# Optimization experiments

Measured on AMD Instinct MI355X. Metric: run time of the kernel, lower is better.

Reference implementation:

```python
import jax, jax.numpy as jnp
import numpy as np

D_MODEL = 2048
N_HEADS = 16
D_HEAD = D_MODEL // N_HEADS
B, S = 4, 2048


def setup_inputs() -> dict:
    key = jax.random.key(0)
    ks = jax.random.split(key, 5)
    scale = 1.0 / np.sqrt(D_MODEL)
    return {
        "x": jax.random.normal(ks[0], (B, S, D_MODEL), dtype=jnp.float32),
        "w_qkv": jax.random.normal(ks[1], (D_MODEL, 3 * D_MODEL), dtype=jnp.float32) * scale,
        "b_qkv": jax.random.normal(ks[2], (3 * D_MODEL,), dtype=jnp.float32) * 0.01,
        "w_out": jax.random.normal(ks[3], (D_MODEL, D_MODEL), dtype=jnp.float32) * scale,
        "b_out": jax.random.normal(ks[4], (D_MODEL,), dtype=jnp.float32) * 0.01,
    }


def reference(x, w_qkv, b_qkv, w_out, b_out):
    b, s, d = x.shape
    qkv = x @ w_qkv + b_qkv                      # [b, s, 3d]
    q, k, v = jnp.split(qkv, 3, axis=-1)
    # [b, h, s, dh]
    q = q.reshape(b, s, N_HEADS, D_HEAD).transpose(0, 2, 1, 3)
    k = k.reshape(b, s, N_HEADS, D_HEAD).transpose(0, 2, 1, 3)
    v = v.reshape(b, s, N_HEADS, D_HEAD).transpose(0, 2, 1, 3)
    # past_kv is None -> s_past == s
    scale = 1.0 / np.sqrt(D_HEAD).astype(np.float32)
    scores = jnp.einsum("bhqd,bhkd->bhqk", q, k) * scale  # [b, h, s, s]
    # causal mask: disallow j > i (diagonal = 1 + s_past - s = 1)
    causal = jnp.tril(jnp.ones((s, s), dtype=bool))
    scores = jnp.where(causal, scores, jnp.float32(-jnp.inf))
    attn = jax.nn.softmax(scores, axis=-1)
    out = jnp.einsum("bhqk,bhkd->bhqd", attn, v)          # [b, h, s, dh]
    out = out.transpose(0, 2, 1, 3).reshape(b, s, d)
    out = out @ w_out + b_out
    return out, k, v
```

## Files before the change

### kernel.cpp

```cpp
#include <hip/hip_runtime.h>
#include <hip/hip_bf16.h>
#include <cstdint>

typedef unsigned short u16;
typedef unsigned int u32;
typedef __attribute__((ext_vector_type(4))) float f32x4;
typedef __attribute__((ext_vector_type(8))) __bf16 bf16x8;

#define DEVFN static __device__ __forceinline__

constexpr int Bb = 4, S = 2048, Dm = 2048, H = 16, DH = 128;
constexpr int M  = Bb * S;
constexpr int N3 = 3 * Dm;
constexpr float ATTN_SCALE = 0.088388347648318447f;
constexpr float LOG2E = 1.4426950408889634f;

DEVFN u16 f2bf(float f) {
  union { float f; u32 u; } v; v.f = f;
  u32 u = v.u;
  return (u16)((u + 0x7fffu + ((u >> 16) & 1u)) >> 16);
}

DEVFN void async16(const void* g, void* l) {
  __builtin_amdgcn_global_load_lds(
      (__attribute__((address_space(1))) unsigned int*)(g),
      (__attribute__((address_space(3))) unsigned int*)(l), 16, 0, 0);
}


__global__ __launch_bounds__(256) void k_cvt_bf16(const float* __restrict__ in,
                                                  u16* __restrict__ out, int n) {
  int i = (blockIdx.x * 256 + threadIdx.x) * 4;
  if (i < n) {
    float4 f = *(const float4*)(in + i);
    ushort4 o;
    o.x = f2bf(f.x); o.y = f2bf(f.y); o.z = f2bf(f.z); o.w = f2bf(f.w);
    *(ushort4*)(out + i) = o;
  }
}

__global__ __launch_bounds__(256) void k_transpose_bf16(const float* __restrict__ in,
                                                        u16* __restrict__ out,
                                                        int R, int C) {
  __shared__ float tile[32][33];
  int c0 = blockIdx.x * 32, r0 = blockIdx.y * 32;
  int tx = threadIdx.x & 31, ty = threadIdx.x >> 5;
#pragma unroll
  for (int i = 0; i < 4; i++)
    tile[ty + 8 * i][tx] = in[(size_t)(r0 + ty + 8 * i) * C + c0 + tx];
  __syncthreads();
#pragma unroll
  for (int i = 0; i < 4; i++)
    out[(size_t)(c0 + ty + 8 * i) * R + r0 + tx] = f2bf(tile[tx][ty + 8 * i]);
}


#define RA(buf, half) ((buf) * 65536 + (half) * 16384)
#define RB(buf, half) ((buf) * 65536 + 32768 + (half) * 16384)

DEVFN void stage_half(const u16* __restrict__ g, int grow0, int K, int vtile,
                      char* lds, int region, int tid) {
#pragma unroll
  for (int j = 0; j < 2; j++) {
    int L = j * 8192 + tid * 16;
    int row = L >> 7;
    int col = (((L & 127) ^ ((row & 7) << 4)) >> 1) + vtile * 64;
    async16(g + (size_t)(grow0 + row) * K + col,
            lds + region + j * 8192 + (tid & ~63) * 16);
  }
}

template <int BUF, int MSUB>
DEVFN void ldA(const char* lds, int wm, int lrow, int lkg, bf16x8 af[4][2]) {
#pragma unroll
  for (int mi = 0; mi < 4; mi++)
#pragma unroll
    for (int kk = 0; kk < 2; kk++) {
      int row = MSUB * 64 + mi * 16 + lrow;
      af[mi][kk] = *(const bf16x8*)(lds + RA(BUF, 0) + wm * 16384 + row * 128 +
                                    ((kk * 64 + lkg * 16) ^ ((row & 7) << 4)));
    }
}

template <int BUF, int NSUB>
DEVFN void ldB(const char* lds, int wn, int lrow, int lkg, bf16x8 bfr[2][2]) {
#pragma unroll
  for (int ni = 0; ni < 2; ni++)
#pragma unroll
    for (int kk = 0; kk < 2; kk++) {
      int row = (wn & 1) * 64 + NSUB * 32 + ni * 16 + lrow;
      bfr[ni][kk] = *(const bf16x8*)(lds + RB(BUF, 0) + (wn >> 1) * 16384 +
                                     row * 128 +
                                     ((kk * 64 + lkg * 16) ^ ((row & 7) << 4)));
    }
}

template <int MSUB, int NSUB>
DEVFN void mmq(f32x4 acc[8][4], bf16x8 af[4][2], bf16x8 bfr[2][2]) {
  __builtin_amdgcn_s_setprio(1);
#pragma unroll
  for (int kk = 0; kk < 2; kk++)
#pragma unroll
    for (int mi = 0; mi < 4; mi++)
#pragma unroll
      for (int ni = 0; ni < 2; ni++)
        acc[MSUB * 4 + mi][NSUB * 2 + ni] = __builtin_amdgcn_mfma_f32_16x16x32_bf16(
            af[mi][kk], bfr[ni][kk], acc[MSUB * 4 + mi][NSUB * 2 + ni], 0, 0, 0);
  __builtin_amdgcn_s_setprio(0);
}

#define BARRIER() __builtin_amdgcn_s_barrier()
#define LGK0() asm volatile("s_waitcnt lgkmcnt(0)" ::: "memory")
#define VM4() asm volatile("s_waitcnt vmcnt(4)" ::: "memory")

template <int MODE>
__global__ __launch_bounds__(512, 2) void k_gemm(
    const u16* __restrict__ A, const u16* __restrict__ BT,
    const float* __restrict__ bias, float* __restrict__ Cf,
    u16* __restrict__ q_bf, u16* __restrict__ k_bf, u16* __restrict__ v_bfT,
    int K, int N) {
  __shared__ __align__(16) char lds[131072];
  const int tid = threadIdx.x;
  const int wid = tid >> 6, lane = tid & 63;
  const int wm = wid >> 2, wn = wid & 3;
  const int lrow = lane & 15, lkg = lane >> 4;

  const int bid = blockIdx.x;
  const int xcd = bid & 7;
  const int i = bid >> 3;
  const int r = i & 15;
  const int j = i >> 4;
  const int tm0 = (xcd * 4 + (r >> 2)) << 8;
  const int tn0 = (j * 4 + (r & 3)) << 8;

  const int NT = K >> 6;

  f32x4 acc[8][4] = {};

  stage_half(A, tm0,       K, 0, lds, RA(0, 0), tid);
  stage_half(BT, tn0,      K, 0, lds, RB(0, 0), tid);
  stage_half(A, tm0 + 128, K, 0, lds, RA(0, 1), tid);
  stage_half(BT, tn0 + 128,K, 0, lds, RB(0, 1), tid);
  stage_half(A, tm0,       K, 1, lds, RA(1, 0), tid);
  stage_half(BT, tn0,      K, 1, lds, RB(1, 0), tid);
  VM4();
  BARRIER();

  for (int u = 0; u < NT; u += 2) {
    const int v2 = (u + 2 < NT) ? u + 2 : 0;
    const int v3 = (u + 3 < NT) ? u + 3 : 0;
    bf16x8 af[4][2], b0[2][2], b1[2][2];

    ldA<0, 0>(lds, wm, lrow, lkg, af);
    ldB<0, 0>(lds, wn, lrow, lkg, b0);
    stage_half(BT, tn0 + 128, K, u + 1, lds, RB(1, 1), tid);
    BARRIER(); LGK0();
    mmq<0, 0>(acc, af, b0);
    BARRIER();

    ldB<0, 1>(lds, wn, lrow, lkg, b1);
    stage_half(A, tm0 + 128, K, u + 1, lds, RA(1, 1), tid);
    BARRIER(); LGK0();
    mmq<0, 1>(acc, af, b1);
    BARRIER();

    ldA<0, 1>(lds, wm, lrow, lkg, af);
    stage_half(BT, tn0, K, v2, lds, RB(0, 0), tid);
    BARRIER(); LGK0();
    mmq<1, 0>(acc, af, b0);
    BARRIER();

    stage_half(A, tm0, K, v2, lds, RA(0, 0), tid);
    VM4();
    BARRIER();
    mmq<1, 1>(acc, af, b1);
    BARRIER();

    ldA<1, 0>(lds, wm, lrow, lkg, af);
    ldB<1, 0>(lds, wn, lrow, lkg, b0);
    stage_half(A, tm0 + 128, K, v2, lds, RA(0, 1), tid);
    BARRIER(); LGK0();
    mmq<0, 0>(acc, af, b0);
    BARRIER();

    ldB<1, 1>(lds, wn, lrow, lkg, b1);
    stage_half(BT, tn0 + 128, K, v2, lds, RB(0, 1), tid);
    BARRIER(); LGK0();
    mmq<0, 1>(acc, af, b1);
    BARRIER();

    ldA<1, 1>(lds, wm, lrow, lkg, af);
    stage_half(BT, tn0, K, v3, lds, RB(1, 0), tid);
    BARRIER(); LGK0();
    mmq<1, 0>(acc, af, b0);
    BARRIER();

    stage_half(A, tm0, K, v3, lds, RA(1, 0), tid);
    VM4();
    BARRIER();
    mmq<1, 1>(acc, af, b1);
    BARRIER();
  }

  if (MODE == 0) {
#pragma unroll
    for (int mig = 0; mig < 8; mig++) {
      int row = tm0 + wm * 128 + (mig >> 2) * 64 + (mig & 3) * 16 + lkg * 4;
#pragma unroll
      for (int nig = 0; nig < 4; nig++) {
        int col = tn0 + wn * 64 + (nig >> 1) * 32 + (nig & 1) * 16 + lrow;
        float bv = bias[col];
#pragma unroll
        for (int r2 = 0; r2 < 4; r2++)
          Cf[(size_t)(row + r2) * N + col] = acc[mig][nig][r2] + bv;
      }
    }
  } else {
#pragma unroll
    for (int mig = 0; mig < 8; mig++) {
      int row = tm0 + wm * 128 + (mig >> 2) * 64 + (mig & 3) * 16 + lkg * 4;
#pragma unroll
      for (int nig = 0; nig < 4; nig++) {
        int n = tn0 + wn * 64 + (nig >> 1) * 32 + (nig & 1) * 16 + lrow;
        float bv = bias[n];
        int type = n >> 11;
        int d = n & 2047;
        int h = d >> 7, dh = d & 127;
#pragma unroll
        for (int r2 = 0; r2 < 4; r2++) {
          int rr = row + r2;
          int b = rr >> 11, s = rr & 2047;
          float val = acc[mig][nig][r2] + bv;
          size_t idx = ((size_t)(b * H + h) * S + s) * DH + dh;
          if (type == 0) {
            q_bf[idx] = f2bf(val * ATTN_SCALE);
          } else if (type == 1) {
            Cf[(size_t)M * Dm + idx] = val;
            k_bf[idx] = f2bf(val);
          } else {
            Cf[(size_t)2 * M * Dm + idx] = val;
            v_bfT[((size_t)(b * H + h) * DH + dh) * S + s] = f2bf(val);
          }
        }
      }
    }
  }
}

__global__ __launch_bounds__(256, 2) void k_attn(const u16* __restrict__ q_bf,
                                                 const u16* __restrict__ k_bf,
                                                 const u16* __restrict__ v_bfT,
                                                 u16* __restrict__ attn_bf) {
  __shared__ u16 ldsK[2][64 * 128];
  __shared__ u16 ldsV[2][128 * 64];
  __shared__ u16 ldsP[4][32 * 64];

  const int tid = threadIdx.x;
  const int wid = tid >> 6, lane = tid & 63;
  const int lrow = lane & 15, lkg = lane >> 4;

  const int bid = blockIdx.x;
  const int xcd = bid & 7;
  const int ii = bid >> 3;
  const int bh = xcd * 8 + (ii >> 4);
  const int qi = 15 - (ii & 15);
  const int b = bh >> 4, h = bh & 15;
  const int wq0 = qi * 128 + wid * 32;
  const int swz = (lrow & 7) << 4;

  const u16* qp = q_bf + (size_t)bh * S * DH;
  const u16* kp = k_bf + (size_t)bh * S * DH;
  const u16* vp = v_bfT + (size_t)bh * DH * S;

  bf16x8 qf[2][4];
#pragma unroll
  for (int qt = 0; qt < 2; qt++)
#pragma unroll
    for (int kk = 0; kk < 4; kk++)
      qf[qt][kk] = *(const bf16x8*)(qp + (size_t)(wq0 + qt * 16 + lrow) * DH +
                                    kk * 32 + lkg * 8);

  float mr[2][4], lr[2][4];
#pragma unroll
  for (int qt = 0; qt < 2; qt++)
#pragma unroll
    for (int r = 0; r < 4; r++) { mr[qt][r] = -1e30f; lr[qt][r] = 0.f; }
  f32x4 oacc[2][8] = {};

  const int nkb = qi * 2 + 2;

  auto stage = [&](int kb, int buf) {
#pragma unroll
    for (int i = 0; i < 4; i++) {
      int L = i * 4096 + wid * 1024 + lane * 16;
      int krow = L >> 8, kch = (L >> 4) & 15;
      async16(kp + (size_t)(kb * 64 + krow) * DH + ((kch ^ (krow & 7)) * 8),
              (char*)ldsK[buf] + L);
      int vd = L >> 7, vch = (L >> 4) & 7;
      async16(vp + (size_t)vd * S + kb * 64 + ((vch ^ (vd & 7)) * 8),
              (char*)ldsV[buf] + L);
    }
  };

  stage(0, 0);
  asm volatile("s_waitcnt vmcnt(0)" ::: "memory");
  __builtin_amdgcn_s_barrier();

  int cur = 0;
  for (int kb = 0; kb < nkb; kb++) {
    if (kb + 1 < nkb) stage(kb + 1, cur ^ 1);

    if (kb * 64 <= wq0 + 31) {
      const u16* Kc = ldsK[cur];
      const u16* Vc = ldsV[cur];
      f32x4 sacc[2][4] = {};
      __builtin_amdgcn_s_setprio(1);
#pragma unroll
      for (int kt = 0; kt < 4; kt++)
#pragma unroll
        for (int kk = 0; kk < 4; kk++) {
          bf16x8 kf = *(const bf16x8*)((const char*)Kc +
                        (kt * 16 + lrow) * 256 + ((kk * 64 + lkg * 16) ^ swz));
          sacc[0][kt] = __builtin_amdgcn_mfma_f32_16x16x32_bf16(qf[0][kk], kf,
                                                                sacc[0][kt], 0, 0, 0);
          sacc[1][kt] = __builtin_amdgcn_mfma_f32_16x16x32_bf16(qf[1][kk], kf,
                                                                sacc[1][kt], 0, 0, 0);
        }
      __builtin_amdgcn_s_setprio(0);

      if (kb * 64 + 63 > wq0) {
#pragma unroll
        for (int qt = 0; qt < 2; qt++)
#pragma unroll
          for (int kt = 0; kt < 4; kt++) {
            int k = kb * 64 + kt * 16 + lrow;
#pragma unroll
            for (int r = 0; r < 4; r++)
              if (k > wq0 + qt * 16 + lkg * 4 + r) sacc[qt][kt][r] = -1e30f;
          }
      }

      float pm[2][4];
#pragma unroll
      for (int qt = 0; qt < 2; qt++)
#pragma unroll
        for (int r = 0; r < 4; r++)
          pm[qt][r] = fmaxf(fmaxf(sacc[qt][0][r], sacc[qt][1][r]),
                            fmaxf(sacc[qt][2][r], sacc[qt][3][r]));
#pragma unroll
      for (int off = 1; off < 16; off <<= 1)
#pragma unroll
        for (int qt = 0; qt < 2; qt++)
#pragma unroll
          for (int r = 0; r < 4; r++)
            pm[qt][r] = fmaxf(pm[qt][r], __shfl_xor(pm[qt][r], off, 64));

      float dmax = pm[0][0] - mr[0][0];
#pragma unroll
      for (int qt = 0; qt < 2; qt++)
#pragma unroll
        for (int r = 0; r < 4; r++)
          dmax = fmaxf(dmax, pm[qt][r] - mr[qt][r]);
      if (!__all(dmax <= 8.0f)) {
        float sc[2][4];
#pragma unroll
        for (int qt = 0; qt < 2; qt++)
#pragma unroll
          for (int r = 0; r < 4; r++) {
            float mn = fmaxf(mr[qt][r], pm[qt][r]);
            sc[qt][r] = exp2f((mr[qt][r] - mn) * LOG2E);
            mr[qt][r] = mn;
            lr[qt][r] *= sc[qt][r];
          }
#pragma unroll
        for (int qt = 0; qt < 2; qt++)
#pragma unroll
          for (int nd = 0; nd < 8; nd++)
#pragma unroll
            for (int r = 0; r < 4; r++) oacc[qt][nd][r] *= sc[qt][r];
      }

      float rs[2][4] = {};
#pragma unroll
      for (int qt = 0; qt < 2; qt++)
#pragma unroll
        for (int kt = 0; kt < 4; kt++)
#pragma unroll
          for (int r = 0; r < 4; r++) {
            float p = exp2f((sacc[qt][kt][r] - mr[qt][r]) * LOG2E);
            rs[qt][r] += p;
            int prow = qt * 16 + lkg * 4 + r;
            *(u16*)((char*)ldsP[wid] + prow * 128 +
                    (((kt * 16 + lrow) * 2) ^ ((prow & 7) << 4))) = f2bf(p);
          }
#pragma unroll
      for (int off = 1; off < 16; off <<= 1)
#pragma unroll
        for (int qt = 0; qt < 2; qt++)
#pragma unroll
          for (int r = 0; r < 4; r++)
            rs[qt][r] += __shfl_xor(rs[qt][r], off, 64);
#pragma unroll
      for (int qt = 0; qt < 2; qt++)
#pragma unroll
        for (int r = 0; r < 4; r++)
          lr[qt][r] += rs[qt][r];

      asm volatile("s_waitcnt lgkmcnt(0)" ::: "memory");
      bf16x8 pf[2][2];
#pragma unroll
      for (int qt = 0; qt < 2; qt++)
#pragma unroll
        for (int kk = 0; kk < 2; kk++)
          pf[qt][kk] = *(const bf16x8*)((const char*)ldsP[wid] +
                         (qt * 16 + lrow) * 128 + ((kk * 64 + lkg * 16) ^ swz));
      __builtin_amdgcn_s_setprio(1);
#pragma unroll
      for (int nd = 0; nd < 8; nd++) {
        bf16x8 vf0 = *(const bf16x8*)((const char*)Vc +
                       (nd * 16 + lrow) * 128 + ((lkg * 16) ^ swz));
        bf16x8 vf1 = *(const bf16x8*)((const char*)Vc +
                       (nd * 16 + lrow) * 128 + ((64 + lkg * 16) ^ swz));
#pragma unroll
        for (int qt = 0; qt < 2; qt++) {
          oacc[qt][nd] = __builtin_amdgcn_mfma_f32_16x16x32_bf16(pf[qt][0], vf0,
                                                                 oacc[qt][nd], 0, 0, 0);
          oacc[qt][nd] = __builtin_amdgcn_mfma_f32_16x16x32_bf16(pf[qt][1], vf1,
                                                                 oacc[qt][nd], 0, 0, 0);
        }
      }
      __builtin_amdgcn_s_setprio(0);
    }

    asm volatile("s_waitcnt vmcnt(0)" ::: "memory");
    __builtin_amdgcn_s_barrier();
    cur ^= 1;
  }

#pragma unroll
  for (int qt = 0; qt < 2; qt++) {
    float inv[4];
#pragma unroll
    for (int r = 0; r < 4; r++) inv[r] = 1.0f / lr[qt][r];
#pragma unroll
    for (int nd = 0; nd < 8; nd++)
#pragma unroll
      for (int r = 0; r < 4; r++) {
        int q = wq0 + qt * 16 + lkg * 4 + r;
        size_t idx = ((size_t)(b * S + q) * H + h) * DH + nd * 16 + lrow;
        attn_bf[idx] = f2bf(oacc[qt][nd][r] * inv[r]);
      }
  }
}


extern "C" void kernel_launch(void* const* d_in, const int* in_sizes, int n_in,
                              void* d_out, int out_size, void* d_ws, size_t ws_size,
                              hipStream_t stream) {
  const float* x     = (const float*)d_in[0];
  const float* w_qkv = (const float*)d_in[1];
  const float* b_qkv = (const float*)d_in[2];
  const float* w_out = (const float*)d_in[3];
  const float* b_out = (const float*)d_in[4];
  float* out = (float*)d_out;

  char* ws = (char*)d_ws;
  u16* x_bf    = (u16*)ws; ws += (size_t)M * Dm * 2;
  u16* wqkvT   = (u16*)ws; ws += (size_t)N3 * Dm * 2;
  u16* woutT   = (u16*)ws; ws += (size_t)Dm * Dm * 2;
  u16* q_bf    = (u16*)ws; ws += (size_t)M * Dm * 2;
  u16* k_bf    = (u16*)ws; ws += (size_t)M * Dm * 2;
  u16* v_bfT   = (u16*)ws; ws += (size_t)M * Dm * 2;
  u16* attn_bf = (u16*)ws; ws += (size_t)M * Dm * 2;

  k_cvt_bf16<<<(M * Dm) / 1024, 256, 0, stream>>>(x, x_bf, M * Dm);
  k_transpose_bf16<<<dim3(N3 / 32, Dm / 32), 256, 0, stream>>>(w_qkv, wqkvT, Dm, N3);
  k_transpose_bf16<<<dim3(Dm / 32, Dm / 32), 256, 0, stream>>>(w_out, woutT, Dm, Dm);

  k_gemm<1><<<(N3 / 256) * (M / 256), 512, 0, stream>>>(
      x_bf, wqkvT, b_qkv, out, q_bf, k_bf, v_bfT, Dm, N3);

  k_attn<<<S / 128 * Bb * H, 256, 0, stream>>>(q_bf, k_bf, v_bfT, attn_bf);

  k_gemm<0><<<(Dm / 256) * (M / 256), 512, 0, stream>>>(
      attn_bf, woutT, b_out, out, nullptr, nullptr, nullptr, Dm, Dm);
}
```

Measured before the change: 549.9 us.

## Restructure GEMM main loop with hoisted A fragments and pointer-increment staging

The GEMM main loop now loads both A sub-tiles from LDS once per buffer instead of twice. It uses precomputed per-thread global pointers that advance by 64 elements, replacing per-call address math. K is fixed at compile time, prologue staging is reordered with a deeper vmcnt wait, and the out-of-range wraparound prefetch is removed in favour of a final vmcnt(0) drain. The goal is fewer LDS reads and less integer address overhead, at the cost of more registers for A fragments and a late prefetch that may read past the tile end.

Measured after the change: 559.9 us. No clear change (+1.8%).

```diff
diff --git a/kernel.cpp b/kernel.cpp
--- a/kernel.cpp
+++ b/kernel.cpp
@@ -12,6 +12,7 @@
 constexpr int Bb = 4, S = 2048, Dm = 2048, H = 16, DH = 128;
 constexpr int M  = Bb * S;
 constexpr int N3 = 3 * Dm;
+constexpr int KK = 2048;
 constexpr float ATTN_SCALE = 0.088388347648318447f;
 constexpr float LOG2E = 1.4426950408889634f;
 
@@ -58,68 +59,71 @@
 #define RA(buf, half) ((buf) * 65536 + (half) * 16384)
 #define RB(buf, half) ((buf) * 65536 + 32768 + (half) * 16384)
 
-DEVFN void stage_half(const u16* __restrict__ g, int grow0, int K, int vtile,
-                      char* lds, int region, int tid) {
-#pragma unroll
-  for (int j = 0; j < 2; j++) {
-    int L = j * 8192 + tid * 16;
-    int row = L >> 7;
-    int col = (((L & 127) ^ ((row & 7) << 4)) >> 1) + vtile * 64;
-    async16(g + (size_t)(grow0 + row) * K + col,
-            lds + region + j * 8192 + (tid & ~63) * 16);
-  }
-}
-
-template <int BUF, int MSUB>
-DEVFN void ldA(const char* lds, int wm, int lrow, int lkg, bf16x8 af[4][2]) {
-#pragma unroll
-  for (int mi = 0; mi < 4; mi++)
-#pragma unroll
-    for (int kk = 0; kk < 2; kk++) {
-      int row = MSUB * 64 + mi * 16 + lrow;
-      af[mi][kk] = *(const bf16x8*)(lds + RA(BUF, 0) + wm * 16384 + row * 128 +
-                                    ((kk * 64 + lkg * 16) ^ ((row & 7) << 4)));
-    }
-}
-
-template <int BUF, int NSUB>
-DEVFN void ldB(const char* lds, int wn, int lrow, int lkg, bf16x8 bfr[2][2]) {
-#pragma unroll
-  for (int ni = 0; ni < 2; ni++)
-#pragma unroll
-    for (int kk = 0; kk < 2; kk++) {
-      int row = (wn & 1) * 64 + NSUB * 32 + ni * 16 + lrow;
-      bfr[ni][kk] = *(const bf16x8*)(lds + RB(BUF, 0) + (wn >> 1) * 16384 +
-                                     row * 128 +
-                                     ((kk * 64 + lkg * 16) ^ ((row & 7) << 4)));
-    }
-}
-
-template <int MSUB, int NSUB>
-DEVFN void mmq(f32x4 acc[8][4], bf16x8 af[4][2], bf16x8 bfr[2][2]) {
-  __builtin_amdgcn_s_setprio(1);
-#pragma unroll
-  for (int kk = 0; kk < 2; kk++)
-#pragma unroll
-    for (int mi = 0; mi < 4; mi++)
-#pragma unroll
-      for (int ni = 0; ni < 2; ni++)
-        acc[MSUB * 4 + mi][NSUB * 2 + ni] = __builtin_amdgcn_mfma_f32_16x16x32_bf16(
-            af[mi][kk], bfr[ni][kk], acc[MSUB * 4 + mi][NSUB * 2 + ni], 0, 0, 0);
-  __builtin_amdgcn_s_setprio(0);
-}
-
 #define BARRIER() __builtin_amdgcn_s_barrier()
 #define LGK0() asm volatile("s_waitcnt lgkmcnt(0)" ::: "memory")
-#define VM4() asm volatile("s_waitcnt vmcnt(4)" ::: "memory")
+#define VM6() asm volatile("s_waitcnt vmcnt(6)" ::: "memory")
+#define VM0() asm volatile("s_waitcnt vmcnt(0)" ::: "memory")
+
+template <int BUF>
+DEVFN void ldAall(const char* lds, int wm, int lrow, int lkg, bf16x8 af[2][4][2]) {
+  const char* base = lds + RA(BUF, 0) + wm * 16384;
+  const int sw = (lrow & 7) << 4;
+#pragma unroll
+  for (int ms = 0; ms < 2; ms++)
+#pragma unroll
+    for (int mi = 0; mi < 4; mi++) {
+      int row = ms * 64 + mi * 16 + lrow;
+#pragma unroll
+      for (int kk = 0; kk < 2; kk++)
+        af[ms][mi][kk] = *(const bf16x8*)(base + row * 128 +
+                                          ((kk * 64 + lkg * 16) ^ sw));
+    }
+}
+
+template <int BUF, int NS>
+DEVFN void ldB(const char* lds, int wn, int lrow, int lkg, bf16x8 b[2][2]) {
+  const char* base = lds + RB(BUF, 0) + (wn >> 1) * 16384;
+  const int sw = (lrow & 7) << 4;
+#pragma unroll
+  for (int ni = 0; ni < 2; ni++) {
+    int row = (wn & 1) * 64 + NS * 32 + ni * 16 + lrow;
+#pragma unroll
+    for (int kk = 0; kk < 2; kk++)
+      b[ni][kk] = *(const bf16x8*)(base + row * 128 +
+                                   ((kk * 64 + lkg * 16) ^ sw));
+  }
+}
+
+template <int MS, int NS>
+DEVFN void mmq(f32x4 acc[8][4], bf16x8 af[4][2], bf16x8 b[2][2]) {
+  __builtin_amdgcn_s_setprio(1);
+#pragma unroll
+  for (int kk = 0; kk < 2; kk++)
+#pragma unroll
+    for (int mi = 0; mi < 4; mi++)
+#pragma unroll
+      for (int ni = 0; ni < 2; ni++)
+        acc[MS * 4 + mi][NS * 2 + ni] = __builtin_amdgcn_mfma_f32_16x16x32_bf16(
+            af[mi][kk], b[ni][kk], acc[MS * 4 + mi][NS * 2 + ni], 0, 0, 0);
+  __builtin_amdgcn_s_setprio(0);
+}
+
+#define STAGE0(ptr, region)                                             \
+  {                                                                     \
+    const u16* _q = (ptr);                                              \
+    async16(_q, ldsc + (region) + dstoff);                              \
+    async16(_q + (size_t)64 * KK, ldsc + (region) + 8192 + dstoff);     \
+  }
+#define STAGE(p, region) { STAGE0(p, region); p += 64; }
 
 template <int MODE>
 __global__ __launch_bounds__(512, 2) void k_gemm(
     const u16* __restrict__ A, const u16* __restrict__ BT,
     const float* __restrict__ bias, float* __restrict__ Cf,
     u16* __restrict__ q_bf, u16* __restrict__ k_bf, u16* __restrict__ v_bfT,
-    int K, int N) {
+    int N) {
   __shared__ __align__(16) char lds[131072];
+  char* ldsc = lds;
   const int tid = threadIdx.x;
   const int wid = tid >> 6, lane = tid & 63;
   const int wm = wid >> 2, wn = wid & 3;
@@ -133,74 +137,85 @@
   const int tm0 = (xcd * 4 + (r >> 2)) << 8;
   const int tn0 = (j * 4 + (r & 3)) << 8;
 
-  const int NT = K >> 6;
+  const int NT = KK >> 6;
+
+  const int srow = tid >> 3;
+  const int scol = (((tid & 7) * 16) ^ ((srow & 7) << 4)) >> 1;
+  const int dstoff = (tid & ~63) * 16;
+  const u16* bA0 = A + (size_t)(tm0 + srow) * KK + scol;
+  const u16* bA1 = A + (size_t)(tm0 + 128 + srow) * KK + scol;
+  const u16* bB0 = BT + (size_t)(tn0 + srow) * KK + scol;
+  const u16* bB1 = BT + (size_t)(tn0 + 128 + srow) * KK + scol;
 
   f32x4 acc[8][4] = {};
 
-  stage_half(A, tm0,       K, 0, lds, RA(0, 0), tid);
-  stage_half(BT, tn0,      K, 0, lds, RB(0, 0), tid);
-  stage_half(A, tm0 + 128, K, 0, lds, RA(0, 1), tid);
-  stage_half(BT, tn0 + 128,K, 0, lds, RB(0, 1), tid);
-  stage_half(A, tm0,       K, 1, lds, RA(1, 0), tid);
-  stage_half(BT, tn0,      K, 1, lds, RB(1, 0), tid);
-  VM4();
+  STAGE0(bA0, RA(0, 0));
+  STAGE0(bA1, RA(0, 1));
+  STAGE0(bB0, RB(0, 0));
+  STAGE0(bB1, RB(0, 1));
+  STAGE0(bA0 + 64, RA(1, 0));
+  STAGE0(bA1 + 64, RA(1, 1));
+  STAGE0(bB0 + 64, RB(1, 0));
+  VM6();
   BARRIER();
 
-  for (int u = 0; u < NT; u += 2) {
-    const int v2 = (u + 2 < NT) ? u + 2 : 0;
-    const int v3 = (u + 3 < NT) ? u + 3 : 0;
-    bf16x8 af[4][2], b0[2][2], b1[2][2];
-
-    ldA<0, 0>(lds, wm, lrow, lkg, af);
-    ldB<0, 0>(lds, wn, lrow, lkg, b0);
-    stage_half(BT, tn0 + 128, K, u + 1, lds, RB(1, 1), tid);
+  const u16* pB1 = bB1 + 64;
+  const u16* pA0 = bA0 + 128;
+  const u16* pA1 = bA1 + 128;
+  const u16* pB0 = bB0 + 128;
+
+  for (int it = 0; it < NT / 2; it++) {
+    bf16x8 af[2][4][2], b0[2][2], b1[2][2];
+
+    ldAall<0>(ldsc, wm, lrow, lkg, af);
+    ldB<0, 0>(ldsc, wn, lrow, lkg, b0);
+    STAGE(pB1, RB(1, 1));
     BARRIER(); LGK0();
-    mmq<0, 0>(acc, af, b0);
-    BARRIER();
-
-    ldB<0, 1>(lds, wn, lrow, lkg, b1);
-    stage_half(A, tm0 + 128, K, u + 1, lds, RA(1, 1), tid);
+    mmq<0, 0>(acc, af[0], b0);
+    BARRIER();
+
+    ldB<0, 1>(ldsc, wn, lrow, lkg, b1);
+    STAGE(pA0, RA(0, 0));
     BARRIER(); LGK0();
-    mmq<0, 1>(acc, af, b1);
-    BARRIER();
-
-    ldA<0, 1>(lds, wm, lrow, lkg, af);
-    stage_half(BT, tn0, K, v2, lds, RB(0, 0), tid);
+    mmq<0, 1>(acc, af[0], b1);
+    BARRIER();
+
+    STAGE(pA1, RA(0, 1));
+    BARRIER();
+    mmq<1, 0>(acc, af[1], b0);
+    BARRIER();
+
+    STAGE(pB0, RB(0, 0));
+    VM6();
+    BARRIER();
+    mmq<1, 1>(acc, af[1], b1);
+    BARRIER();
+
+    ldAall<1>(ldsc, wm, lrow, lkg, af);
+    ldB<1, 0>(ldsc, wn, lrow, lkg, b0);
+    STAGE(pB1, RB(0, 1));
     BARRIER(); LGK0();
-    mmq<1, 0>(acc, af, b0);
-    BARRIER();
-
-    stage_half(A, tm0, K, v2, lds, RA(0, 0), tid);
-    VM4();
-    BARRIER();
-    mmq<1, 1>(acc, af, b1);
-    BARRIER();
-
-    ldA<1, 0>(lds, wm, lrow, lkg, af);
-    ldB<1, 0>(lds, wn, lrow, lkg, b0);
-    stage_half(A, tm0 + 128, K, v2, lds, RA(0, 1), tid);
+    mmq<0, 0>(acc, af[0], b0);
+    BARRIER();
+
+    ldB<1, 1>(ldsc, wn, lrow, lkg, b1);
+    STAGE(pA0, RA(1, 0));
     BARRIER(); LGK0();
-    mmq<0, 0>(acc, af, b0);
-    BARRIER();
-
-    ldB<1, 1>(lds, wn, lrow, lkg, b1);
-    stage_half(BT, tn0 + 128, K, v2, lds, RB(0, 1), tid);
-    BARRIER(); LGK0();
-    mmq<0, 1>(acc, af, b1);
-    BARRIER();
-
-    ldA<1, 1>(lds, wm, lrow, lkg, af);
-    stage_half(BT, tn0, K, v3, lds, RB(1, 0), tid);
-    BARRIER(); LGK0();
-    mmq<1, 0>(acc, af, b0);
-    BARRIER();
-
-    stage_half(A, tm0, K, v3, lds, RA(1, 0), tid);
-    VM4();
-    BARRIER();
-    mmq<1, 1>(acc, af, b1);
-    BARRIER();
-  }
+    mmq<0, 1>(acc, af[0], b1);
+    BARRIER();
+
+    STAGE(pA1, RA(1, 1));
+    BARRIER();
+    mmq<1, 0>(acc, af[1], b0);
+    BARRIER();
+
+    STAGE(pB0, RB(1, 0));
+    VM6();
+    BARRIER();
+    mmq<1, 1>(acc, af[1], b1);
+    BARRIER();
+  }
+  VM0();
 
   if (MODE == 0) {
 #pragma unroll
@@ -478,10 +493,10 @@
   k_transpose_bf16<<<dim3(Dm / 32, Dm / 32), 256, 0, stream>>>(w_out, woutT, Dm, Dm);
 
   k_gemm<1><<<(N3 / 256) * (M / 256), 512, 0, stream>>>(
-      x_bf, wqkvT, b_qkv, out, q_bf, k_bf, v_bfT, Dm, N3);
+      x_bf, wqkvT, b_qkv, out, q_bf, k_bf, v_bfT, N3);
 
   k_attn<<<S / 128 * Bb * H, 256, 0, stream>>>(q_bf, k_bf, v_bfT, attn_bf);
 
   k_gemm<0><<<(Dm / 256) * (M / 256), 512, 0, stream>>>(
-      attn_bf, woutT, b_out, out, nullptr, nullptr, nullptr, Dm, Dm);
-}
+      attn_bf, woutT, b_out, out, nullptr, nullptr, nullptr, Dm);
+}
```
